# Kernel optimization log

Hardware: AMD Instinct MI355X
Metric: run time of the kernel (lower is better)

## Reference

```python
import jax, jax.numpy as jnp
import numpy as np

WINDOW_SIZE = 3
SIGMA = 1.5
C1 = 0.01 ** 2
C2 = 0.03 ** 2


def gaussian_window(channel, window_size=WINDOW_SIZE, sigma=SIGMA):
    x = jnp.arange(window_size, dtype=jnp.float32) - window_size // 2
    g1 = jnp.exp(-(x ** 2) / (2.0 * sigma ** 2))
    g1 = g1 / g1.sum()
    g2 = jnp.outer(g1, g1)  # [k, k]
    # depthwise kernel OIHW: [C, 1, k, k]
    return jnp.broadcast_to(g2, (channel, 1, window_size, window_size))


def depthwise_conv(x, window, channel, window_size=WINDOW_SIZE):
    pad = window_size // 2
    return jax.lax.conv_general_dilated(
        x, window,
        window_strides=(1, 1),
        padding=((pad, pad), (pad, pad)),
        dimension_numbers=('NCHW', 'OIHW', 'NCHW'),
        feature_group_count=channel,
    )


def setup_inputs() -> dict:
    key = jax.random.key(0)
    k1, k2 = jax.random.split(key)
    img1 = jax.random.uniform(k1, (32, 3, 512, 512), dtype=jnp.float32)
    img2 = jax.random.uniform(k2, (32, 3, 512, 512), dtype=jnp.float32)
    return {"img1": img1, "img2": img2}


def reference(img1, img2):
    channel = img1.shape[1]
    window = gaussian_window(channel)

    mu1 = depthwise_conv(img1, window, channel)
    mu2 = depthwise_conv(img2, window, channel)
    mu1_sq = mu1 * mu1
    mu2_sq = mu2 * mu2
    mu1_mu2 = mu1 * mu2

    sigma1_sq = depthwise_conv(img1 * img1, window, channel) - mu1_sq
    sigma2_sq = depthwise_conv(img2 * img2, window, channel) - mu2_sq
    sigma12 = depthwise_conv(img1 * img2, window, channel) - mu1_mu2

    ssim_map = ((2.0 * mu1_mu2 + C1) * (2.0 * sigma12 + C2)) / (
        (mu1_sq + mu2_sq + C1) * (sigma1_sq + sigma2_sq + C2))

    # size_sum defaults to True inside ssim() -> scalar sum
    return 1.0 - ssim_map.sum()
```

## Files before the change

kernel.cpp:

```cpp
#include <hip/hip_runtime.h>

#define IMG_H 512
#define IMG_W 512
#define RH 32


typedef float v2f __attribute__((ext_vector_type(2), aligned(8)));

__global__ __launch_bounds__(256) void ssim_main_kernel(
    const float* __restrict__ img1, const float* __restrict__ img2,
    double* __restrict__ partial)
{
    constexpr float W_E = 0.30780133f;
    constexpr float W_C = 0.38439734f;
    constexpr float RW = W_C / W_E;
    constexpr float K2 = W_E * W_E;
    constexpr float C1c = 1e-4f;
    constexpr float C2c = 9e-4f;

    const int t = threadIdx.x;
    const int y0 = blockIdx.x * RH;
    const size_t base = (size_t)blockIdx.y * (size_t)(IMG_H * IMG_W);
    const float* __restrict__ A = img1 + base;
    const float* __restrict__ B = img2 + base;
    const bool has_l = (t > 0);
    const bool has_r = (t < 255);
    const int x = 2 * t;

    float n1[2][3], n2[2][3], nss[2][3], n12[2][3];
    float tsum = 0.0f;

    float a00, a01, a02, a03, b00, b01, b02, b03;
    float a10, a11, a12, a13, b10, b11, b12, b13;

#define LOADROW(AP, BP, OFF) do {                                   \
    const v2f _ma = *(const v2f*)(A + (OFF));                       \
    const v2f _mb = *(const v2f*)(B + (OFF));                       \
    AP##1 = _ma.x; AP##2 = _ma.y; BP##1 = _mb.x; BP##2 = _mb.y;     \
    AP##0 = has_l ? A[(OFF) - 1] : 0.0f;                            \
    AP##3 = has_r ? A[(OFF) + 2] : 0.0f;                            \
    BP##0 = has_l ? B[(OFF) - 1] : 0.0f;                            \
    BP##3 = has_r ? B[(OFF) + 2] : 0.0f;                            \
} while (0)

#define ZEROROW(AP, BP) do {                                        \
    AP##0 = 0.f; AP##1 = 0.f; AP##2 = 0.f; AP##3 = 0.f;             \
    BP##0 = 0.f; BP##1 = 0.f; BP##2 = 0.f; BP##3 = 0.f;             \
} while (0)

#define HPASS(AP, BP, S) do {                                               \
    const float ss0 = __builtin_fmaf(BP##0, BP##0, AP##0 * AP##0);          \
    const float ss1 = __builtin_fmaf(BP##1, BP##1, AP##1 * AP##1);          \
    const float ss2 = __builtin_fmaf(BP##2, BP##2, AP##2 * AP##2);          \
    const float ss3 = __builtin_fmaf(BP##3, BP##3, AP##3 * AP##3);          \
    const float p0 = AP##0 * BP##0, p1 = AP##1 * BP##1;                     \
    const float p2 = AP##2 * BP##2, p3 = AP##3 * BP##3;                     \
    n1[0][S]  = __builtin_fmaf(RW, AP##1, AP##0 + AP##2);                   \
    n1[1][S]  = __builtin_fmaf(RW, AP##2, AP##1 + AP##3);                   \
    n2[0][S]  = __builtin_fmaf(RW, BP##1, BP##0 + BP##2);                   \
    n2[1][S]  = __builtin_fmaf(RW, BP##2, BP##1 + BP##3);                   \
    nss[0][S] = __builtin_fmaf(RW, ss1, ss0 + ss2);                         \
    nss[1][S] = __builtin_fmaf(RW, ss2, ss1 + ss3);                         \
    n12[0][S] = __builtin_fmaf(RW, p1, p0 + p2);                            \
    n12[1][S] = __builtin_fmaf(RW, p2, p1 + p3);                            \
} while (0)

#define VOUT(E0, E1, MID) do {                                              \
    _Pragma("unroll")                                                       \
    for (int c = 0; c < 2; ++c) {                                           \
        const float mu1 = K2 * __builtin_fmaf(RW, n1[c][MID],  n1[c][E0] + n1[c][E1]);  \
        const float mu2 = K2 * __builtin_fmaf(RW, n2[c][MID],  n2[c][E0] + n2[c][E1]);  \
        const float ess = K2 * __builtin_fmaf(RW, nss[c][MID], nss[c][E0] + nss[c][E1]);\
        const float e12 = K2 * __builtin_fmaf(RW, n12[c][MID], n12[c][E0] + n12[c][E1]);\
        const float mu1s = mu1 * mu1, mu2s = mu2 * mu2, m12 = mu1 * mu2;    \
        const float sss = (ess - mu1s) - mu2s;                              \
        const float s12 = e12 - m12;                                        \
        const float num = __builtin_fmaf(2.0f, m12, C1c) *                  \
                          __builtin_fmaf(2.0f, s12, C2c);                   \
        const float den = ((mu1s + mu2s) + C1c) * (sss + C2c);              \
        tsum += num / den;                                                  \
    }                                                                       \
} while (0)

    size_t off = (size_t)y0 * IMG_W + x;

    if (blockIdx.x != 0) LOADROW(a0, b0, off - IMG_W); else ZEROROW(a0, b0);
    LOADROW(a1, b1, off);
    HPASS(a0, b0, 0);
    LOADROW(a0, b0, off + IMG_W);
    HPASS(a1, b1, 1);
    off += 2 * (size_t)IMG_W;

#pragma unroll 1
    for (int g = 0; g < 5; ++g) {
        LOADROW(a1, b1, off); off += IMG_W; HPASS(a0, b0, 2); VOUT(2, 0, 1);
        LOADROW(a0, b0, off); off += IMG_W; HPASS(a1, b1, 0); VOUT(0, 1, 2);
        LOADROW(a1, b1, off); off += IMG_W; HPASS(a0, b0, 1); VOUT(1, 2, 0);
        LOADROW(a0, b0, off); off += IMG_W; HPASS(a1, b1, 2); VOUT(2, 0, 1);
        LOADROW(a1, b1, off); off += IMG_W; HPASS(a0, b0, 0); VOUT(0, 1, 2);
        LOADROW(a0, b0, off); off += IMG_W; HPASS(a1, b1, 1); VOUT(1, 2, 0);
    }

    if (blockIdx.x != (IMG_H / RH - 1)) LOADROW(a1, b1, off); else ZEROROW(a1, b1);
    HPASS(a0, b0, 2); VOUT(2, 0, 1);
    HPASS(a1, b1, 0); VOUT(0, 1, 2);

#undef LOADROW
#undef ZEROROW
#undef HPASS
#undef VOUT

#pragma unroll
    for (int o = 32; o >= 1; o >>= 1)
        tsum += __shfl_xor(tsum, o, 64);

    __shared__ float wpart[4];
    if ((t & 63) == 0) wpart[t >> 6] = tsum;
    __syncthreads();
    if (t == 0) {
        partial[(size_t)blockIdx.y * gridDim.x + blockIdx.x] =
            (double)wpart[0] + (double)wpart[1] +
            (double)wpart[2] + (double)wpart[3];
    }
}

__global__ __launch_bounds__(256) void ssim_fin_kernel(
    const double* __restrict__ partial, float* __restrict__ out, int n)
{
    const int t = threadIdx.x;
    double s = 0.0;
    for (int i = t; i < n; i += 256) s += partial[i];
#pragma unroll
    for (int o = 32; o >= 1; o >>= 1)
        s += __shfl_xor(s, o, 64);
    __shared__ double w[4];
    if ((t & 63) == 0) w[t >> 6] = s;
    __syncthreads();
    if (t == 0)
        out[0] = 1.0f - (float)(w[0] + w[1] + w[2] + w[3]);
}

extern "C" void kernel_launch(void* const* d_in, const int* in_sizes, int n_in,
                              void* d_out, int out_size, void* d_ws, size_t ws_size,
                              hipStream_t stream) {
    const float* img1 = (const float*)d_in[0];
    const float* img2 = (const float*)d_in[1];
    float* out = (float*)d_out;
    double* partial = (double*)d_ws;

    const int planes = in_sizes[0] / (IMG_H * IMG_W);
    const int nblk = IMG_H / RH;

    dim3 grid(nblk, planes);
    ssim_main_kernel<<<grid, 256, 0, stream>>>(img1, img2, partial);
    ssim_fin_kernel<<<1, 256, 0, stream>>>(partial, out, nblk * planes);
}
```

Measured before the change: 225.2 us.

## Fetch horizontal halo via wavefront shuffles and load two rows per step

```diff
diff --git a/kernel.cpp b/kernel.cpp
--- a/kernel.cpp
+++ b/kernel.cpp
@@ -3,6 +3,7 @@
 #define IMG_H 512
 #define IMG_W 512
 #define RH 32
+#define NBX (IMG_H / RH)
 
 
 typedef float v2f __attribute__((ext_vector_type(2), aligned(8)));
@@ -23,96 +24,144 @@
     const size_t base = (size_t)blockIdx.y * (size_t)(IMG_H * IMG_W);
     const float* __restrict__ A = img1 + base;
     const float* __restrict__ B = img2 + base;
-    const bool has_l = (t > 0);
-    const bool has_r = (t < 255);
     const int x = 2 * t;
+
+    const bool isL = ((t & 63) == 0);
+    const bool isR = ((t & 63) == 63);
+    const bool isEdge = isL | isR;
+    const float mE = (t == 0 || t == 255) ? 0.0f : 1.0f;
+    const int hd = isL ? ((t == 0) ? 0 : -1)
+                       : ((t == 255) ? 1 : 2);
 
     float n1[2][3], n2[2][3], nss[2][3], n12[2][3];
     float tsum = 0.0f;
 
-    float a00, a01, a02, a03, b00, b01, b02, b03;
-    float a10, a11, a12, a13, b10, b11, b12, b13;
-
-#define LOADROW(AP, BP, OFF) do {                                   \
-    const v2f _ma = *(const v2f*)(A + (OFF));                       \
-    const v2f _mb = *(const v2f*)(B + (OFF));                       \
-    AP##1 = _ma.x; AP##2 = _ma.y; BP##1 = _mb.x; BP##2 = _mb.y;     \
-    AP##0 = has_l ? A[(OFF) - 1] : 0.0f;                            \
-    AP##3 = has_r ? A[(OFF) + 2] : 0.0f;                            \
-    BP##0 = has_l ? B[(OFF) - 1] : 0.0f;                            \
-    BP##3 = has_r ? B[(OFF) + 2] : 0.0f;                            \
+    v2f zz; zz.x = 0.0f; zz.y = 0.0f;
+
+    v2f Pa0, Pa1, Pb0, Pb1; float PhA0, PhB0, PhA1, PhB1;
+    v2f Qa0, Qa1, Qb0, Qb1; float QhA0, QhB0, QhA1, QhB1;
+
+#define LOADB(PRE, O) do {                                                    \
+    PRE##a0 = *(const v2f*)(A + (O));                                         \
+    PRE##b0 = *(const v2f*)(B + (O));                                         \
+    PRE##a1 = *(const v2f*)(A + (O) + IMG_W);                                 \
+    PRE##b1 = *(const v2f*)(B + (O) + IMG_W);                                 \
+    if (isEdge) {                                                             \
+        PRE##hA0 = (A + (O))[hd];          PRE##hB0 = (B + (O))[hd];          \
+        PRE##hA1 = (A + (O) + IMG_W)[hd];  PRE##hB1 = (B + (O) + IMG_W)[hd];  \
+    }                                                                         \
 } while (0)
 
-#define ZEROROW(AP, BP) do {                                        \
-    AP##0 = 0.f; AP##1 = 0.f; AP##2 = 0.f; AP##3 = 0.f;             \
-    BP##0 = 0.f; BP##1 = 0.f; BP##2 = 0.f; BP##3 = 0.f;             \
+#define HROW(RA, RB, HA, HB, S) do {                                          \
+    float am_ = __shfl_up(RA.y, 1, 64);                                       \
+    float ap_ = __shfl_down(RA.x, 1, 64);                                     \
+    float bm_ = __shfl_up(RB.y, 1, 64);                                       \
+    float bp_ = __shfl_down(RB.x, 1, 64);                                     \
+    const float heA = (HA) * mE, heB = (HB) * mE;                             \
+    am_ = isL ? heA : am_;  ap_ = isR ? heA : ap_;                            \
+    bm_ = isL ? heB : bm_;  bp_ = isR ? heB : bp_;                            \
+    const float a0_ = RA.x, a1_ = RA.y, b0_ = RB.x, b1_ = RB.y;               \
+    const float ss0 = __builtin_fmaf(bm_, bm_, am_ * am_);                    \
+    const float ss1 = __builtin_fmaf(b0_, b0_, a0_ * a0_);                    \
+    const float ss2 = __builtin_fmaf(b1_, b1_, a1_ * a1_);                    \
+    const float ss3 = __builtin_fmaf(bp_, bp_, ap_ * ap_);                    \
+    const float p0 = am_ * bm_, p1 = a0_ * b0_;                               \
+    const float p2 = a1_ * b1_, p3 = ap_ * bp_;                               \
+    n1[0][S]  = __builtin_fmaf(RW, a0_, am_ + a1_);                           \
+    n1[1][S]  = __builtin_fmaf(RW, a1_, a0_ + ap_);                           \
+    n2[0][S]  = __builtin_fmaf(RW, b0_, bm_ + b1_);                           \
+    n2[1][S]  = __builtin_fmaf(RW, b1_, b0_ + bp_);                           \
+    nss[0][S] = __builtin_fmaf(RW, ss1, ss0 + ss2);                           \
+    nss[1][S] = __builtin_fmaf(RW, ss2, ss1 + ss3);                           \
+    n12[0][S] = __builtin_fmaf(RW, p1, p0 + p2);                              \
+    n12[1][S] = __builtin_fmaf(RW, p2, p1 + p3);                              \
 } while (0)
 
-#define HPASS(AP, BP, S) do {                                               \
-    const float ss0 = __builtin_fmaf(BP##0, BP##0, AP##0 * AP##0);          \
-    const float ss1 = __builtin_fmaf(BP##1, BP##1, AP##1 * AP##1);          \
-    const float ss2 = __builtin_fmaf(BP##2, BP##2, AP##2 * AP##2);          \
-    const float ss3 = __builtin_fmaf(BP##3, BP##3, AP##3 * AP##3);          \
-    const float p0 = AP##0 * BP##0, p1 = AP##1 * BP##1;                     \
-    const float p2 = AP##2 * BP##2, p3 = AP##3 * BP##3;                     \
-    n1[0][S]  = __builtin_fmaf(RW, AP##1, AP##0 + AP##2);                   \
-    n1[1][S]  = __builtin_fmaf(RW, AP##2, AP##1 + AP##3);                   \
-    n2[0][S]  = __builtin_fmaf(RW, BP##1, BP##0 + BP##2);                   \
-    n2[1][S]  = __builtin_fmaf(RW, BP##2, BP##1 + BP##3);                   \
-    nss[0][S] = __builtin_fmaf(RW, ss1, ss0 + ss2);                         \
-    nss[1][S] = __builtin_fmaf(RW, ss2, ss1 + ss3);                         \
-    n12[0][S] = __builtin_fmaf(RW, p1, p0 + p2);                            \
-    n12[1][S] = __builtin_fmaf(RW, p2, p1 + p3);                            \
-} while (0)
-
-#define VOUT(E0, E1, MID) do {                                              \
-    _Pragma("unroll")                                                       \
-    for (int c = 0; c < 2; ++c) {                                           \
+#define VOUT(E0, E1, MID) do {                                                \
+    _Pragma("unroll")                                                         \
+    for (int c = 0; c < 2; ++c) {                                             \
         const float mu1 = K2 * __builtin_fmaf(RW, n1[c][MID],  n1[c][E0] + n1[c][E1]);  \
         const float mu2 = K2 * __builtin_fmaf(RW, n2[c][MID],  n2[c][E0] + n2[c][E1]);  \
         const float ess = K2 * __builtin_fmaf(RW, nss[c][MID], nss[c][E0] + nss[c][E1]);\
         const float e12 = K2 * __builtin_fmaf(RW, n12[c][MID], n12[c][E0] + n12[c][E1]);\
-        const float mu1s = mu1 * mu1, mu2s = mu2 * mu2, m12 = mu1 * mu2;    \
-        const float sss = (ess - mu1s) - mu2s;                              \
-        const float s12 = e12 - m12;                                        \
-        const float num = __builtin_fmaf(2.0f, m12, C1c) *                  \
-                          __builtin_fmaf(2.0f, s12, C2c);                   \
-        const float den = ((mu1s + mu2s) + C1c) * (sss + C2c);              \
-        tsum += num / den;                                                  \
-    }                                                                       \
+        const float mu1s = mu1 * mu1, mu2s = mu2 * mu2, m12 = mu1 * mu2;      \
+        const float sss = (ess - mu1s) - mu2s;                                \
+        const float s12 = e12 - m12;                                          \
+        const float num = __builtin_fmaf(2.0f, m12, C1c) *                    \
+                          __builtin_fmaf(2.0f, s12, C2c);                     \
+        const float den = ((mu1s + mu2s) + C1c) * (sss + C2c);                \
+        tsum += num / den;                                                    \
+    }                                                                         \
 } while (0)
 
-    size_t off = (size_t)y0 * IMG_W + x;
-
-    if (blockIdx.x != 0) LOADROW(a0, b0, off - IMG_W); else ZEROROW(a0, b0);
-    LOADROW(a1, b1, off);
-    HPASS(a0, b0, 0);
-    LOADROW(a0, b0, off + IMG_W);
-    HPASS(a1, b1, 1);
-    off += 2 * (size_t)IMG_W;
+    const size_t off = (size_t)y0 * IMG_W + x;
+
+    if (blockIdx.x != 0) {
+        Pa0 = *(const v2f*)(A + off - IMG_W);
+        Pb0 = *(const v2f*)(B + off - IMG_W);
+        if (isEdge) { PhA0 = (A + off - IMG_W)[hd]; PhB0 = (B + off - IMG_W)[hd]; }
+    } else { Pa0 = zz; Pb0 = zz; PhA0 = 0.f; PhB0 = 0.f; }
+    Pa1 = *(const v2f*)(A + off);
+    Pb1 = *(const v2f*)(B + off);
+    if (isEdge) { PhA1 = (A + off)[hd]; PhB1 = (B + off)[hd]; }
+
+    size_t o = off + IMG_W;
+
+    LOADB(Q, o); o += 2 * IMG_W;
+    HROW(Pa0, Pb0, PhA0, PhB0, 0);
+    HROW(Pa1, Pb1, PhA1, PhB1, 1);
 
 #pragma unroll 1
-    for (int g = 0; g < 5; ++g) {
-        LOADROW(a1, b1, off); off += IMG_W; HPASS(a0, b0, 2); VOUT(2, 0, 1);
-        LOADROW(a0, b0, off); off += IMG_W; HPASS(a1, b1, 0); VOUT(0, 1, 2);
-        LOADROW(a1, b1, off); off += IMG_W; HPASS(a0, b0, 1); VOUT(1, 2, 0);
-        LOADROW(a0, b0, off); off += IMG_W; HPASS(a1, b1, 2); VOUT(2, 0, 1);
-        LOADROW(a1, b1, off); off += IMG_W; HPASS(a0, b0, 0); VOUT(0, 1, 2);
-        LOADROW(a0, b0, off); off += IMG_W; HPASS(a1, b1, 1); VOUT(1, 2, 0);
+    for (int g = 0; g < 2; ++g) {
+        LOADB(P, o); o += 2 * IMG_W;
+        HROW(Qa0, Qb0, QhA0, QhB0, 2); VOUT(2, 0, 1);
+        HROW(Qa1, Qb1, QhA1, QhB1, 0); VOUT(0, 1, 2);
+        LOADB(Q, o); o += 2 * IMG_W;
+        HROW(Pa0, Pb0, PhA0, PhB0, 1); VOUT(1, 2, 0);
+        HROW(Pa1, Pb1, PhA1, PhB1, 2); VOUT(2, 0, 1);
+        LOADB(P, o); o += 2 * IMG_W;
+        HROW(Qa0, Qb0, QhA0, QhB0, 0); VOUT(0, 1, 2);
+        HROW(Qa1, Qb1, QhA1, QhB1, 1); VOUT(1, 2, 0);
+        LOADB(Q, o); o += 2 * IMG_W;
+        HROW(Pa0, Pb0, PhA0, PhB0, 2); VOUT(2, 0, 1);
+        HROW(Pa1, Pb1, PhA1, PhB1, 0); VOUT(0, 1, 2);
+        LOADB(P, o); o += 2 * IMG_W;
+        HROW(Qa0, Qb0, QhA0, QhB0, 1); VOUT(1, 2, 0);
+        HROW(Qa1, Qb1, QhA1, QhB1, 2); VOUT(2, 0, 1);
+        LOADB(Q, o); o += 2 * IMG_W;
+        HROW(Pa0, Pb0, PhA0, PhB0, 0); VOUT(0, 1, 2);
+        HROW(Pa1, Pb1, PhA1, PhB1, 1); VOUT(1, 2, 0);
     }
 
-    if (blockIdx.x != (IMG_H / RH - 1)) LOADROW(a1, b1, off); else ZEROROW(a1, b1);
-    HPASS(a0, b0, 2); VOUT(2, 0, 1);
-    HPASS(a1, b1, 0); VOUT(0, 1, 2);
-
-#undef LOADROW
-#undef ZEROROW
-#undef HPASS
+    LOADB(P, o); o += 2 * IMG_W;
+    HROW(Qa0, Qb0, QhA0, QhB0, 2); VOUT(2, 0, 1);
+    HROW(Qa1, Qb1, QhA1, QhB1, 0); VOUT(0, 1, 2);
+
+    LOADB(Q, o); o += 2 * IMG_W;
+    HROW(Pa0, Pb0, PhA0, PhB0, 1); VOUT(1, 2, 0);
+    HROW(Pa1, Pb1, PhA1, PhB1, 2); VOUT(2, 0, 1);
+
+    Pa0 = *(const v2f*)(A + o);
+    Pb0 = *(const v2f*)(B + o);
+    if (isEdge) { PhA0 = (A + o)[hd]; PhB0 = (B + o)[hd]; }
+    if (blockIdx.x != NBX - 1) {
+        Pa1 = *(const v2f*)(A + o + IMG_W);
+        Pb1 = *(const v2f*)(B + o + IMG_W);
+        if (isEdge) { PhA1 = (A + o + IMG_W)[hd]; PhB1 = (B + o + IMG_W)[hd]; }
+    } else { Pa1 = zz; Pb1 = zz; PhA1 = 0.f; PhB1 = 0.f; }
+    HROW(Qa0, Qb0, QhA0, QhB0, 0); VOUT(0, 1, 2);
+    HROW(Qa1, Qb1, QhA1, QhB1, 1); VOUT(1, 2, 0);
+
+    HROW(Pa0, Pb0, PhA0, PhB0, 2); VOUT(2, 0, 1);
+    HROW(Pa1, Pb1, PhA1, PhB1, 0); VOUT(0, 1, 2);
+
+#undef LOADB
+#undef HROW
 #undef VOUT
 
 #pragma unroll
-    for (int o = 32; o >= 1; o >>= 1)
-        tsum += __shfl_xor(tsum, o, 64);
+    for (int sft = 32; sft >= 1; sft >>= 1)
+        tsum += __shfl_xor(tsum, sft, 64);
 
     __shared__ float wpart[4];
     if ((t & 63) == 0) wpart[t >> 6] = tsum;
@@ -149,9 +198,8 @@
     double* partial = (double*)d_ws;
 
     const int planes = in_sizes[0] / (IMG_H * IMG_W);
-    const int nblk = IMG_H / RH;
-
-    dim3 grid(nblk, planes);
+
+    dim3 grid(NBX, planes);
     ssim_main_kernel<<<grid, 256, 0, stream>>>(img1, img2, partial);
-    ssim_fin_kernel<<<1, 256, 0, stream>>>(partial, out, nblk * planes);
+    ssim_fin_kernel<<<1, 256, 0, stream>>>(partial, out, NBX * planes);
 }
```

Result: no change. 226.9 us (+0.7%).

## Use float4 row loads with wavefront shuffles for horizontal halo exchange

Applied to the files above, without the earlier changes.

```diff
diff --git a/kernel.cpp b/kernel.cpp
--- a/kernel.cpp
+++ b/kernel.cpp
@@ -3,11 +3,12 @@
 #define IMG_H 512
 #define IMG_W 512
 #define RH 32
+#define NBX (IMG_H / RH)
 
 
-typedef float v2f __attribute__((ext_vector_type(2), aligned(8)));
+typedef float v4f __attribute__((ext_vector_type(4), aligned(16)));
 
-__global__ __launch_bounds__(256) void ssim_main_kernel(
+__global__ __launch_bounds__(128) void ssim_main_kernel(
     const float* __restrict__ img1, const float* __restrict__ img2,
     double* __restrict__ partial)
 {
@@ -23,87 +24,110 @@
     const size_t base = (size_t)blockIdx.y * (size_t)(IMG_H * IMG_W);
     const float* __restrict__ A = img1 + base;
     const float* __restrict__ B = img2 + base;
-    const bool has_l = (t > 0);
-    const bool has_r = (t < 255);
-    const int x = 2 * t;
+    const int x = 4 * t;
 
-    float n1[2][3], n2[2][3], nss[2][3], n12[2][3];
+    const bool isL = ((t & 63) == 0);
+    const bool isR = ((t & 63) == 63);
+    const bool isEdge = isL | isR;
+    const float mE = (t == 0 || t == 127) ? 0.0f : 1.0f;
+    const int hd = isL ? ((t == 0) ? 0 : -1)
+                       : ((t == 127) ? 1 : 4);
+
+    float n1[4][3], n2[4][3], nss[4][3], n12[4][3];
     float tsum = 0.0f;
 
-    float a00, a01, a02, a03, b00, b01, b02, b03;
-    float a10, a11, a12, a13, b10, b11, b12, b13;
+    v4f Pa, Pb; float PhA, PhB;
+    v4f Qa, Qb; float QhA, QhB;
 
-#define LOADROW(AP, BP, OFF) do {                                   \
-    const v2f _ma = *(const v2f*)(A + (OFF));                       \
-    const v2f _mb = *(const v2f*)(B + (OFF));                       \
-    AP##1 = _ma.x; AP##2 = _ma.y; BP##1 = _mb.x; BP##2 = _mb.y;     \
-    AP##0 = has_l ? A[(OFF) - 1] : 0.0f;                            \
-    AP##3 = has_r ? A[(OFF) + 2] : 0.0f;                            \
-    BP##0 = has_l ? B[(OFF) - 1] : 0.0f;                            \
-    BP##3 = has_r ? B[(OFF) + 2] : 0.0f;                            \
+#define LOADROW(V, OFF) do {                                                  \
+    V##a = *(const v4f*)(A + (OFF));                                          \
+    V##b = *(const v4f*)(B + (OFF));                                          \
+    if (isEdge) { V##hA = (A + (OFF))[hd]; V##hB = (B + (OFF))[hd]; }         \
 } while (0)
 
-#define ZEROROW(AP, BP) do {                                        \
-    AP##0 = 0.f; AP##1 = 0.f; AP##2 = 0.f; AP##3 = 0.f;             \
-    BP##0 = 0.f; BP##1 = 0.f; BP##2 = 0.f; BP##3 = 0.f;             \
+#define ZEROROW(V) do {                                                       \
+    V##a.x = 0.f; V##a.y = 0.f; V##a.z = 0.f; V##a.w = 0.f;                   \
+    V##b.x = 0.f; V##b.y = 0.f; V##b.z = 0.f; V##b.w = 0.f;                   \
+    V##hA = 0.f;  V##hB = 0.f;                                                \
 } while (0)
 
-#define HPASS(AP, BP, S) do {                                               \
-    const float ss0 = __builtin_fmaf(BP##0, BP##0, AP##0 * AP##0);          \
-    const float ss1 = __builtin_fmaf(BP##1, BP##1, AP##1 * AP##1);          \
-    const float ss2 = __builtin_fmaf(BP##2, BP##2, AP##2 * AP##2);          \
-    const float ss3 = __builtin_fmaf(BP##3, BP##3, AP##3 * AP##3);          \
-    const float p0 = AP##0 * BP##0, p1 = AP##1 * BP##1;                     \
-    const float p2 = AP##2 * BP##2, p3 = AP##3 * BP##3;                     \
-    n1[0][S]  = __builtin_fmaf(RW, AP##1, AP##0 + AP##2);                   \
-    n1[1][S]  = __builtin_fmaf(RW, AP##2, AP##1 + AP##3);                   \
-    n2[0][S]  = __builtin_fmaf(RW, BP##1, BP##0 + BP##2);                   \
-    n2[1][S]  = __builtin_fmaf(RW, BP##2, BP##1 + BP##3);                   \
-    nss[0][S] = __builtin_fmaf(RW, ss1, ss0 + ss2);                         \
-    nss[1][S] = __builtin_fmaf(RW, ss2, ss1 + ss3);                         \
-    n12[0][S] = __builtin_fmaf(RW, p1, p0 + p2);                            \
-    n12[1][S] = __builtin_fmaf(RW, p2, p1 + p3);                            \
+#define HPASS(V, S) do {                                                      \
+    float al_ = __shfl_up(V##a.w, 1, 64);                                     \
+    float ar_ = __shfl_down(V##a.x, 1, 64);                                   \
+    float bl_ = __shfl_up(V##b.w, 1, 64);                                     \
+    float br_ = __shfl_down(V##b.x, 1, 64);                                   \
+    const float heA = V##hA * mE, heB = V##hB * mE;                           \
+    al_ = isL ? heA : al_;  ar_ = isR ? heA : ar_;                            \
+    bl_ = isL ? heB : bl_;  br_ = isR ? heB : br_;                            \
+    const float ea0 = al_, ea1 = V##a.x, ea2 = V##a.y;                        \
+    const float ea3 = V##a.z, ea4 = V##a.w, ea5 = ar_;                        \
+    const float eb0 = bl_, eb1 = V##b.x, eb2 = V##b.y;                        \
+    const float eb3 = V##b.z, eb4 = V##b.w, eb5 = br_;                        \
+    const float ss0 = __builtin_fmaf(eb0, eb0, ea0 * ea0);                    \
+    const float ss1 = __builtin_fmaf(eb1, eb1, ea1 * ea1);                    \
+    const float ss2 = __builtin_fmaf(eb2, eb2, ea2 * ea2);                    \
+    const float ss3 = __builtin_fmaf(eb3, eb3, ea3 * ea3);                    \
+    const float ss4 = __builtin_fmaf(eb4, eb4, ea4 * ea4);                    \
+    const float ss5 = __builtin_fmaf(eb5, eb5, ea5 * ea5);                    \
+    const float p0 = ea0 * eb0, p1 = ea1 * eb1, p2 = ea2 * eb2;               \
+    const float p3 = ea3 * eb3, p4 = ea4 * eb4, p5 = ea5 * eb5;               \
+    n1[0][S]  = __builtin_fmaf(RW, ea1, ea0 + ea2);                           \
+    n1[1][S]  = __builtin_fmaf(RW, ea2, ea1 + ea3);                           \
+    n1[2][S]  = __builtin_fmaf(RW, ea3, ea2 + ea4);                           \
+    n1[3][S]  = __builtin_fmaf(RW, ea4, ea3 + ea5);                           \
+    n2[0][S]  = __builtin_fmaf(RW, eb1, eb0 + eb2);                           \
+    n2[1][S]  = __builtin_fmaf(RW, eb2, eb1 + eb3);                           \
+    n2[2][S]  = __builtin_fmaf(RW, eb3, eb2 + eb4);                           \
+    n2[3][S]  = __builtin_fmaf(RW, eb4, eb3 + eb5);                           \
+    nss[0][S] = __builtin_fmaf(RW, ss1, ss0 + ss2);                           \
+    nss[1][S] = __builtin_fmaf(RW, ss2, ss1 + ss3);                           \
+    nss[2][S] = __builtin_fmaf(RW, ss3, ss2 + ss4);                           \
+    nss[3][S] = __builtin_fmaf(RW, ss4, ss3 + ss5);                           \
+    n12[0][S] = __builtin_fmaf(RW, p1, p0 + p2);                              \
+    n12[1][S] = __builtin_fmaf(RW, p2, p1 + p3);                              \
+    n12[2][S] = __builtin_fmaf(RW, p3, p2 + p4);                              \
+    n12[3][S] = __builtin_fmaf(RW, p4, p3 + p5);                              \
 } while (0)
 
-#define VOUT(E0, E1, MID) do {                                              \
-    _Pragma("unroll")                                                       \
-    for (int c = 0; c < 2; ++c) {                                           \
+#define VOUT(E0, E1, MID) do {                                                \
+    _Pragma("unroll")                                                         \
+    for (int c = 0; c < 4; ++c) {                                             \
         const float mu1 = K2 * __builtin_fmaf(RW, n1[c][MID],  n1[c][E0] + n1[c][E1]);  \
         const float mu2 = K2 * __builtin_fmaf(RW, n2[c][MID],  n2[c][E0] + n2[c][E1]);  \
         const float ess = K2 * __builtin_fmaf(RW, nss[c][MID], nss[c][E0] + nss[c][E1]);\
         const float e12 = K2 * __builtin_fmaf(RW, n12[c][MID], n12[c][E0] + n12[c][E1]);\
-        const float mu1s = mu1 * mu1, mu2s = mu2 * mu2, m12 = mu1 * mu2;    \
-        const float sss = (ess - mu1s) - mu2s;                              \
-        const float s12 = e12 - m12;                                        \
-        const float num = __builtin_fmaf(2.0f, m12, C1c) *                  \
-                          __builtin_fmaf(2.0f, s12, C2c);                   \
-        const float den = ((mu1s + mu2s) + C1c) * (sss + C2c);              \
-        tsum += num / den;                                                  \
-    }                                                                       \
+        const float mu1s = mu1 * mu1, mu2s = mu2 * mu2, m12 = mu1 * mu2;      \
+        const float sss = (ess - mu1s) - mu2s;                                \
+        const float s12 = e12 - m12;                                          \
+        const float num = __builtin_fmaf(2.0f, m12, C1c) *                    \
+                          __builtin_fmaf(2.0f, s12, C2c);                     \
+        const float den = ((mu1s + mu2s) + C1c) * (sss + C2c);                \
+        tsum += num / den;                                                    \
+    }                                                                         \
 } while (0)
 
     size_t off = (size_t)y0 * IMG_W + x;
 
-    if (blockIdx.x != 0) LOADROW(a0, b0, off - IMG_W); else ZEROROW(a0, b0);
-    LOADROW(a1, b1, off);
-    HPASS(a0, b0, 0);
-    LOADROW(a0, b0, off + IMG_W);
-    HPASS(a1, b1, 1);
+    if (blockIdx.x != 0) LOADROW(P, off - IMG_W); else ZEROROW(P);
+    LOADROW(Q, off);
+    HPASS(P, 0);
+    LOADROW(P, off + IMG_W);
+    HPASS(Q, 1);
     off += 2 * (size_t)IMG_W;
 
 #pragma unroll 1
     for (int g = 0; g < 5; ++g) {
-        LOADROW(a1, b1, off); off += IMG_W; HPASS(a0, b0, 2); VOUT(2, 0, 1);
-        LOADROW(a0, b0, off); off += IMG_W; HPASS(a1, b1, 0); VOUT(0, 1, 2);
-        LOADROW(a1, b1, off); off += IMG_W; HPASS(a0, b0, 1); VOUT(1, 2, 0);
-        LOADROW(a0, b0, off); off += IMG_W; HPASS(a1, b1, 2); VOUT(2, 0, 1);
-        LOADROW(a1, b1, off); off += IMG_W; HPASS(a0, b0, 0); VOUT(0, 1, 2);
-        LOADROW(a0, b0, off); off += IMG_W; HPASS(a1, b1, 1); VOUT(1, 2, 0);
+        LOADROW(Q, off); off += IMG_W; HPASS(P, 2); VOUT(2, 0, 1);
+        LOADROW(P, off); off += IMG_W; HPASS(Q, 0); VOUT(0, 1, 2);
+        LOADROW(Q, off); off += IMG_W; HPASS(P, 1); VOUT(1, 2, 0);
+        LOADROW(P, off); off += IMG_W; HPASS(Q, 2); VOUT(2, 0, 1);
+        LOADROW(Q, off); off += IMG_W; HPASS(P, 0); VOUT(0, 1, 2);
+        LOADROW(P, off); off += IMG_W; HPASS(Q, 1); VOUT(1, 2, 0);
     }
 
-    if (blockIdx.x != (IMG_H / RH - 1)) LOADROW(a1, b1, off); else ZEROROW(a1, b1);
-    HPASS(a0, b0, 2); VOUT(2, 0, 1);
-    HPASS(a1, b1, 0); VOUT(0, 1, 2);
+    if (blockIdx.x != NBX - 1) LOADROW(Q, off); else ZEROROW(Q);
+    HPASS(P, 2); VOUT(2, 0, 1);
+    HPASS(Q, 0); VOUT(0, 1, 2);
 
 #undef LOADROW
 #undef ZEROROW
@@ -114,13 +138,12 @@
     for (int o = 32; o >= 1; o >>= 1)
         tsum += __shfl_xor(tsum, o, 64);
 
-    __shared__ float wpart[4];
+    __shared__ float wpart[2];
     if ((t & 63) == 0) wpart[t >> 6] = tsum;
     __syncthreads();
     if (t == 0) {
         partial[(size_t)blockIdx.y * gridDim.x + blockIdx.x] =
-            (double)wpart[0] + (double)wpart[1] +
-            (double)wpart[2] + (double)wpart[3];
+            (double)wpart[0] + (double)wpart[1];
     }
 }
 
@@ -149,9 +172,8 @@
     double* partial = (double*)d_ws;
 
     const int planes = in_sizes[0] / (IMG_H * IMG_W);
-    const int nblk = IMG_H / RH;
 
-    dim3 grid(nblk, planes);
-    ssim_main_kernel<<<grid, 256, 0, stream>>>(img1, img2, partial);
-    ssim_fin_kernel<<<1, 256, 0, stream>>>(partial, out, nblk * planes);
+    dim3 grid(NBX, planes);
+    ssim_main_kernel<<<grid, 128, 0, stream>>>(img1, img2, partial);
+    ssim_fin_kernel<<<1, 256, 0, stream>>>(partial, out, NBX * planes);
 }
```

New measurement: 224.8 us. Within noise of the previous version (-0.2%).
